# Performance work log

Hardware: AMD Instinct MI355X
Metric: run time of the kernel (lower is better)

The kernel has to match this reference:

```python
import jax, jax.numpy as jnp
jax.config.update("jax_enable_x64", True)
import numpy as np

BUCKETS = 2147483647  # max int32, as in fused_project call sites
HALF = BUCKETS >> 1
NGRAM_SIZE = 3
# sgnn partition boundaries: indices = [i*(i+1)/2 * P for i in range(n)] + [proj], P=112
IDX = [0, 112, 336, 672]


def _project(sig, mask, seeds):
    """One SgnnProjection partition.

    sig:   [B, M] int64 hash signatures in [0, BUCKETS) (padded ragged rows)
    mask:  [B, M] bool validity of each padded slot (ragged row structure)
    seeds: [H] int64 hash seeds
    returns [B, H] float32
    """
    # value = floormod(abs(sig * seed), buckets); center to [-half, half]
    v = jnp.abs(sig[None, :, :] * seeds[:, None, None]) % BUCKETS  # [H, B, M]
    v = v - jnp.where(v > HALF, BUCKETS, 0)
    vf = v.astype(jnp.float32) * mask[None].astype(jnp.float32)
    counts = jnp.maximum(mask.sum(-1), 1).astype(jnp.float32)  # [B], ragged row lengths
    mean = vf.sum(-1) / counts[None]  # [H, B]  (ragged reduce_mean)
    return (mean / HALF).T  # [B, H]


def setup_inputs() -> dict:
    key = jax.random.key(0)
    k1, k2, k3 = jax.random.split(key, 3)
    signatures = jax.random.randint(k1, (NGRAM_SIZE, 1024, 128), 0, BUCKETS, dtype=jnp.int64)
    mask = jax.random.bernoulli(k2, 0.7, (NGRAM_SIZE, 1024, 128))
    hash_seed = jax.random.randint(k3, (IDX[-1],), 1, BUCKETS, dtype=jnp.int64)
    return {"signatures": signatures, "mask": mask, "hash_seed": hash_seed}


def reference(signatures, mask, hash_seed):
    outs = [
        _project(signatures[i], mask[i], hash_seed[IDX[i]:IDX[i + 1]])
        for i in range(NGRAM_SIZE)
    ]
    return jnp.concatenate(outs, axis=-1).astype(jnp.float32)  # [B, 672]
```

## Files before the change

kernel.cpp:

```cpp
#include <hip/hip_runtime.h>


#define M31    2147483647u
#define HALF_B 1073741823u

__global__ __launch_bounds__(64) void sgnn_prep_kernel(
    const int* __restrict__ sig,
    const int* __restrict__ mask,
    unsigned* __restrict__ msig,
    float* __restrict__ invc)
{
    const int row = blockIdx.x;
    const int t   = threadIdx.x;
    const int g0  = row * 128 + t;
    const int g1  = g0 + 64;
    const int mk0 = mask[g0], mk1 = mask[g1];
    msig[g0] = mk0 ? (unsigned)sig[g0] : 0u;
    msig[g1] = mk1 ? (unsigned)sig[g1] : 0u;
    const unsigned long long b0 = __ballot(mk0 != 0);
    const unsigned long long b1 = __ballot(mk1 != 0);
    if (t == 0) {
        int c = __popcll(b0) + __popcll(b1);
        if (c < 1) c = 1;
        invc[row] = 1.0f / ((float)c * 1073741823.0f);
    }
}

__device__ __forceinline__ void acc_elem(unsigned v, unsigned seed,
                                         unsigned long long& sum, unsigned& q) {
    const unsigned long long p2 =
        (unsigned long long)v * (unsigned long long)seed + (unsigned long long)HALF_B;
    const unsigned lo = (unsigned)p2;
    const unsigned hi = (unsigned)(p2 >> 32);
    const unsigned s  = __builtin_amdgcn_alignbit(hi, lo, 31) + (lo & 0x7FFFFFFFu);
    q   += (s >= M31);
    sum += s;
}

__global__ __launch_bounds__(256, 8) void sgnn_main_kernel(
    const unsigned* __restrict__ msig,
    const float* __restrict__ invc,
    const int* __restrict__ seeds,
    float* __restrict__ out,
    int nbatch)
{
    const unsigned t = blockIdx.x * 256u + threadIdx.x;
    const unsigned x = t >> 5;
    const unsigned b = (x * 99865u) >> 21;
    const unsigned h = t - 672u * b;
    const int p = (h < 112u) ? 0 : (h < 336u) ? 1 : 2;

    const unsigned* __restrict__ rp = msig + (unsigned)(p * nbatch + b) * 128u;
    const unsigned seed = (unsigned)seeds[h];

    unsigned long long sum0 = 0, sum1 = 0;
    unsigned q0 = 0, q1 = 0;

    #pragma unroll 2
    for (int mm = 0; mm < 128; mm += 16) {
        const uint4 a = *(const uint4*)(rp + mm);
        const uint4 c = *(const uint4*)(rp + mm + 4);
        const uint4 d = *(const uint4*)(rp + mm + 8);
        const uint4 e = *(const uint4*)(rp + mm + 12);
        acc_elem(a.x, seed, sum0, q0); acc_elem(a.y, seed, sum1, q1);
        acc_elem(a.z, seed, sum0, q0); acc_elem(a.w, seed, sum1, q1);
        acc_elem(c.x, seed, sum0, q0); acc_elem(c.y, seed, sum1, q1);
        acc_elem(c.z, seed, sum0, q0); acc_elem(c.w, seed, sum1, q1);
        acc_elem(d.x, seed, sum0, q0); acc_elem(d.y, seed, sum1, q1);
        acc_elem(d.z, seed, sum0, q0); acc_elem(d.w, seed, sum1, q1);
        acc_elem(e.x, seed, sum0, q0); acc_elem(e.y, seed, sum1, q1);
        acc_elem(e.z, seed, sum0, q0); acc_elem(e.w, seed, sum1, q1);
    }

    const long long centered = (long long)(sum0 + sum1)
                             - (long long)(q0 + q1) * 2147483647LL
                             - 128LL * 1073741823LL;
    out[t] = (float)centered * invc[p * nbatch + b];
}

extern "C" void kernel_launch(void* const* d_in, const int* in_sizes, int n_in,
                              void* d_out, int out_size, void* d_ws, size_t ws_size,
                              hipStream_t stream) {
    const int* sig   = (const int*)d_in[0];
    const int* mask  = (const int*)d_in[1];
    const int* seeds = (const int*)d_in[2];
    float* out = (float*)d_out;

    const int nbatch = in_sizes[0] / (3 * 128);
    unsigned* msig = (unsigned*)d_ws;
    float* invc = (float*)((char*)d_ws + (size_t)(3 * nbatch * 128) * 4);

    sgnn_prep_kernel<<<dim3(3 * nbatch), dim3(64), 0, stream>>>(sig, mask, msig, invc);
    const int total = nbatch * 672;
    sgnn_main_kernel<<<dim3(total / 256), dim3(256), 0, stream>>>(msig, invc, seeds, out, nbatch);
}
```

Baseline: 81.37 us.

## Compact masked signatures per row and loop only over valid count

The prep kernel now stream-compacts the valid signatures of each row to the front using ballot prefix counts, pads the count up to a multiple of 16 with zeros, and records that padded count. The main kernel loops only to the padded count instead of all 128 slots and subtracts the centering offset for that many elements, skipping about 30% of the masked-out work. The unroll pragma is removed and the occupancy hint in launch bounds is lowered. The loop is now variable-length, and different rows within a wavefront may have different counts, causing divergence.

Measured after the change: 76.53 us. 1.06x faster.

```diff
diff --git a/kernel.cpp b/kernel.cpp
--- a/kernel.cpp
+++ b/kernel.cpp
@@ -8,21 +8,35 @@
     const int* __restrict__ sig,
     const int* __restrict__ mask,
     unsigned* __restrict__ msig,
-    float* __restrict__ invc)
+    float* __restrict__ invc,
+    unsigned* __restrict__ cnt16)
 {
     const int row = blockIdx.x;
     const int t   = threadIdx.x;
     const int g0  = row * 128 + t;
     const int g1  = g0 + 64;
     const int mk0 = mask[g0], mk1 = mask[g1];
-    msig[g0] = mk0 ? (unsigned)sig[g0] : 0u;
-    msig[g1] = mk1 ? (unsigned)sig[g1] : 0u;
+    const unsigned v0 = (unsigned)sig[g0], v1 = (unsigned)sig[g1];
+
     const unsigned long long b0 = __ballot(mk0 != 0);
     const unsigned long long b1 = __ballot(mk1 != 0);
+    const unsigned long long lt = (1ULL << t) - 1ULL;
+    const int c0   = __popcll(b0);
+    const int cnt  = c0 + __popcll(b1);
+    const int pos0 = __popcll(b0 & lt);
+    const int pos1 = c0 + __popcll(b1 & lt);
+
+    const unsigned base = (unsigned)row * 128u;
+    if (mk0) msig[base + pos0] = v0;
+    if (mk1) msig[base + pos1] = v1;
+
+    const int c16 = (cnt + 15) & ~15;
+    if (cnt + t < c16) msig[base + cnt + t] = 0u;
+
     if (t == 0) {
-        int c = __popcll(b0) + __popcll(b1);
-        if (c < 1) c = 1;
-        invc[row] = 1.0f / ((float)c * 1073741823.0f);
+        int c = (cnt < 1) ? 1 : cnt;
+        invc[row]  = 1.0f / ((float)c * 1073741823.0f);
+        cnt16[row] = (unsigned)c16;
     }
 }
 
@@ -37,9 +51,10 @@
     sum += s;
 }
 
-__global__ __launch_bounds__(256, 8) void sgnn_main_kernel(
+__global__ __launch_bounds__(256, 4) void sgnn_main_kernel(
     const unsigned* __restrict__ msig,
     const float* __restrict__ invc,
+    const unsigned* __restrict__ cnt16,
     const int* __restrict__ seeds,
     float* __restrict__ out,
     int nbatch)
@@ -50,14 +65,15 @@
     const unsigned h = t - 672u * b;
     const int p = (h < 112u) ? 0 : (h < 336u) ? 1 : 2;
 
-    const unsigned* __restrict__ rp = msig + (unsigned)(p * nbatch + b) * 128u;
+    const unsigned row = (unsigned)(p * nbatch) + b;
+    const unsigned* __restrict__ rp = msig + row * 128u;
     const unsigned seed = (unsigned)seeds[h];
+    const unsigned n = cnt16[row];
 
     unsigned long long sum0 = 0, sum1 = 0;
     unsigned q0 = 0, q1 = 0;
 
-    #pragma unroll 2
-    for (int mm = 0; mm < 128; mm += 16) {
+    for (unsigned mm = 0; mm < n; mm += 16) {
         const uint4 a = *(const uint4*)(rp + mm);
         const uint4 c = *(const uint4*)(rp + mm + 4);
         const uint4 d = *(const uint4*)(rp + mm + 8);
@@ -74,8 +90,8 @@
 
     const long long centered = (long long)(sum0 + sum1)
                              - (long long)(q0 + q1) * 2147483647LL
-                             - 128LL * 1073741823LL;
-    out[t] = (float)centered * invc[p * nbatch + b];
+                             - (long long)n * 1073741823LL;
+    out[t] = (float)centered * invc[row];
 }
 
 extern "C" void kernel_launch(void* const* d_in, const int* in_sizes, int n_in,
@@ -87,10 +103,12 @@
     float* out = (float*)d_out;
 
     const int nbatch = in_sizes[0] / (3 * 128);
-    unsigned* msig = (unsigned*)d_ws;
-    float* invc = (float*)((char*)d_ws + (size_t)(3 * nbatch * 128) * 4);
+    const int nrows  = 3 * nbatch;
+    unsigned* msig  = (unsigned*)d_ws;
+    float*    invc  = (float*)((char*)d_ws + (size_t)nrows * 128 * 4);
+    unsigned* c16   = (unsigned*)((char*)d_ws + (size_t)nrows * 132 * 4);
 
-    sgnn_prep_kernel<<<dim3(3 * nbatch), dim3(64), 0, stream>>>(sig, mask, msig, invc);
+    sgnn_prep_kernel<<<dim3(nrows), dim3(64), 0, stream>>>(sig, mask, msig, invc, c16);
     const int total = nbatch * 672;
-    sgnn_main_kernel<<<dim3(total / 256), dim3(256), 0, stream>>>(msig, invc, seeds, out, nbatch);
+    sgnn_main_kernel<<<dim3(total / 256), dim3(256), 0, stream>>>(msig, invc, c16, seeds, out, nbatch);
 }
```
